# Kernel optimization log

Measured on AMD Instinct MI355X. Metric: run time of the kernel, lower is better.

## Reference

```python
import jax, jax.numpy as jnp
import numpy as np

B, V, F = 128, 256, 64      # batch, vertices, features-per-vertex
NS, NLR, K, NOUT = 4, 64, 40, 128
F_EFF = 2 * F               # cat_means doubles feature dim


def setup_inputs() -> dict:
    key = jax.random.key(0)
    k0, k1, k2 = jax.random.split(key, 3)
    x = jax.random.normal(k0, (B, V, F), dtype=jnp.float32)
    # f_slr: single Linear(F_EFF, NS+NLR) + ReLU (f_slr_depth=1)
    W_slr = jax.random.normal(k1, (F_EFF, NS + NLR), dtype=jnp.float32) / np.sqrt(F_EFF).astype(np.float32)
    b_slr = jnp.zeros((NS + NLR,), dtype=jnp.float32)
    # f_out: single Linear(F_EFF + 2*NLR, NOUT) + ReLU (f_out_depth=1, 2 agg methods)
    fin = F_EFF + 2 * NLR
    W_out = jax.random.normal(k2, (fin, NOUT), dtype=jnp.float32) / np.sqrt(fin).astype(np.float32)
    b_out = jnp.zeros((NOUT,), dtype=jnp.float32)
    return {"x": x, "W_slr": W_slr, "b_slr": b_slr, "W_out": W_out, "b_out": b_out}


def reference(x, W_slr, b_slr, W_out, b_out):
    # cat_means: append per-event feature means (broadcast over vertices)
    x = jnp.concatenate([x, jnp.broadcast_to(x.mean(axis=1, keepdims=True), x.shape)], axis=-1)  # (B,V,2F)
    slr = jax.nn.relu(x @ W_slr + b_slr)                    # (B,V,NS+NLR)
    s, lr = slr[..., :NS], slr[..., NS:]
    # pairwise squared distances in latent space (potential only needs d^2, so
    # we skip the sqrt: exp(-10*d^2) == exp(-10*d2), and kNN order is identical)
    diff = s[:, :, None, :] - s[:, None, :, :]              # (B,V,V,NS)
    d2 = jnp.sum(diff * diff, axis=-1)                      # (B,V,V)
    _, idx = jax.lax.top_k(-d2, K)                          # (B,V,K) k smallest (incl. self)
    d2k = jnp.take_along_axis(d2, idx, axis=2)              # (B,V,K)
    lr_nb = jax.vmap(lambda l, i: l[i])(lr, idx)            # (B,V,K,NLR)
    v = jnp.exp(-10.0 * d2k)                                # potential exp(-10 d^2)
    ft = lr_nb * v[..., None]                               # (B,V,K,NLR)
    fp = jnp.concatenate([x, ft.mean(axis=2), ft.max(axis=2)], axis=-1)  # (B,V,2F+2NLR)
    return jax.nn.relu(fp @ W_out + b_out)                  # (B,V,NOUT)
```

## Files before the change

kernel.cpp:

```cpp
#include <hip/hip_runtime.h>

constexpr int Bn = 128, Vn = 256, Fn = 64;
constexpr int NSLR = 68, NSn = 4, NLRn = 64;
constexpr int Kn = 40, NOUTn = 128;
constexpr int ROWS = Bn * Vn;
constexpr int KB2 = 192;

typedef __attribute__((ext_vector_type(8))) short short8;
typedef __attribute__((ext_vector_type(4))) float f32x4;

__device__ __forceinline__ int mbcnt64(unsigned long long m) {
  return __builtin_amdgcn_mbcnt_hi((unsigned)(m >> 32),
         __builtin_amdgcn_mbcnt_lo((unsigned)(m & 0xFFFFFFFFull), 0));
}
__device__ __forceinline__ unsigned short rneb(float v) {
  unsigned u = __float_as_uint(v);
  unsigned r = u + 0x7FFFu + ((u >> 16) & 1u);
  return (unsigned short)(r >> 16);
}
__device__ __forceinline__ float bf2f(unsigned short h) {
  return __uint_as_float(((unsigned)h) << 16);
}
#define GL_LDS(gp, lp) __builtin_amdgcn_global_load_lds( \
    (const __attribute__((address_space(1))) void*)(gp), \
    (__attribute__((address_space(3))) void*)(lp), 16, 0, 0)

__global__ __launch_bounds__(256) void kprep(
    const float* __restrict__ x,
    const float* __restrict__ W_slr, const float* __restrict__ b_slr,
    const float* __restrict__ W_out, const float* __restrict__ b_out,
    short* __restrict__ xhi, short* __restrict__ xlo,
    short* __restrict__ wt1h, short* __restrict__ wt1l, short* __restrict__ wt2,
    float* __restrict__ bias1, float* __restrict__ bias2) {
  const int blk = blockIdx.x, t = threadIdx.x;
  if (blk >= Bn) {
    const int col = blk - Bn;
    if (t < 64) {
      float val = (col < NSLR) ? W_slr[t * NSLR + col] : 0.f;
      unsigned short h = rneb(val);
      wt1h[col * 64 + t] = (short)h;
      wt1l[col * 64 + t] = (short)rneb(val - bf2f(h));
    } else {
      int k = t - 64;
      int row = (k < 64) ? k : 64 + k;
      wt2[col * KB2 + k] = (short)rneb(W_out[row * NOUTn + col]);
    }
    return;
  }
  const int b = blk;
  const int f4 = t & 15, vg = t >> 4;
  const float4* xb = (const float4*)(x + (size_t)b * 16384);
  float4 sum = make_float4(0.f, 0.f, 0.f, 0.f);
  for (int i = 0; i < 16; ++i) {
    int v = vg * 16 + i;
    float4 val = xb[v * 16 + f4];
    sum.x += val.x; sum.y += val.y; sum.z += val.z; sum.w += val.w;
    unsigned short h0 = rneb(val.x), h1 = rneb(val.y), h2 = rneb(val.z), h3 = rneb(val.w);
    short4 hi = {(short)h0, (short)h1, (short)h2, (short)h3};
    short4 lo = {(short)rneb(val.x - bf2f(h0)), (short)rneb(val.y - bf2f(h1)),
                 (short)rneb(val.z - bf2f(h2)), (short)rneb(val.w - bf2f(h3))};
    size_t o = (size_t)b * 4096 + v * 16 + f4;
    ((short4*)xhi)[o] = hi;
    ((short4*)xlo)[o] = lo;
  }
  __shared__ float4 ps[16][16];
  __shared__ float xms[64];
  ps[vg][f4] = sum;
  __syncthreads();
  if (t < 16) {
    float4 m = ps[0][t];
    for (int g = 1; g < 16; ++g) {
      float4 v = ps[g][t];
      m.x += v.x; m.y += v.y; m.z += v.z; m.w += v.w;
    }
    m.x *= (1.f / 256.f); m.y *= (1.f / 256.f); m.z *= (1.f / 256.f); m.w *= (1.f / 256.f);
    ((float4*)xms)[t] = m;
  }
  __syncthreads();
  if (t < 128) {
    float acc = b_out[t];
    for (int f = 0; f < 64; ++f) acc = fmaf(xms[f], W_out[(64 + f) * NOUTn + t], acc);
    bias2[b * 128 + t] = acc;
  } else {
    int c = t - 128;
    if (c < NSLR) {
      float acc = b_slr[c];
      for (int f = 0; f < 64; ++f) acc = fmaf(xms[f], W_slr[(64 + f) * NSLR + c], acc);
      bias1[b * 128 + c] = acc;
    }
  }
}

__global__ __launch_bounds__(256) void kgemm1(
    const short* __restrict__ xhi, const short* __restrict__ xlo,
    const short* __restrict__ wt1h, const short* __restrict__ wt1l,
    const float* __restrict__ bias1,
    float* __restrict__ s_ws, unsigned short* __restrict__ lr_bf) {
  __shared__ __align__(16) short Ah[4096], Al[4096], Bh[8192], Bl[1024];
  const int t = threadIdx.x, l = t & 63, w = t >> 6;
  const int wr = w >> 1, wc = w & 1;
  const int rowBase = blockIdx.x * 64;
  const int b = rowBase >> 8;
  const int lr8 = l >> 3, ul = (l & 7) ^ lr8;

#pragma unroll
  for (int rep = 0; rep < 2; ++rep) {
    const int seg = w + rep * 4;
    size_t o = (size_t)(rowBase + seg * 8 + lr8) * 64 + ul * 8;
    GL_LDS(xhi + o, &Ah[seg * 512]);
    GL_LDS(xlo + o, &Al[seg * 512]);
  }
#pragma unroll
  for (int rep = 0; rep < 4; ++rep) {
    const int seg = w + rep * 4;
    size_t o = (size_t)(seg * 8 + lr8) * 64 + ul * 8;
    GL_LDS(wt1h + o, &Bh[seg * 512]);
  }
  if (w < 2) {
    size_t o = (size_t)(w * 8 + lr8) * 64 + ul * 8;
    GL_LDS(wt1l + o, &Bl[w * 512]);
  }
  __syncthreads();

  f32x4 acc[2][4];
#pragma unroll
  for (int mf = 0; mf < 2; ++mf)
#pragma unroll
    for (int nf = 0; nf < 4; ++nf) acc[mf][nf] = (f32x4)(0.f);

#pragma unroll
  for (int ks = 0; ks < 2; ++ks) {
    short8 ah[2], bh[4];
#pragma unroll
    for (int mf = 0; mf < 2; ++mf) {
      int row = wr * 32 + mf * 16 + (l & 15);
      int pu = (ks * 4 + (l >> 4)) ^ (row & 7);
      ah[mf] = *(const short8*)&Ah[row * 64 + pu * 8];
    }
#pragma unroll
    for (int nf = 0; nf < 4; ++nf) {
      int col = wc * 64 + nf * 16 + (l & 15);
      int pu = (ks * 4 + (l >> 4)) ^ (col & 7);
      bh[nf] = *(const short8*)&Bh[col * 64 + pu * 8];
    }
#pragma unroll
    for (int mf = 0; mf < 2; ++mf)
#pragma unroll
      for (int nf = 0; nf < 4; ++nf)
        acc[mf][nf] = __builtin_amdgcn_mfma_f32_16x16x32_bf16(ah[mf], bh[nf], acc[mf][nf], 0, 0, 0);
    if (wc == 0) {
      int col0 = l & 15;
      int puc = (ks * 4 + (l >> 4)) ^ (col0 & 7);
      short8 bl0 = *(const short8*)&Bl[col0 * 64 + puc * 8];
#pragma unroll
      for (int mf = 0; mf < 2; ++mf) {
        int row = wr * 32 + mf * 16 + (l & 15);
        int pu = (ks * 4 + (l >> 4)) ^ (row & 7);
        short8 al = *(const short8*)&Al[row * 64 + pu * 8];
        acc[mf][0] = __builtin_amdgcn_mfma_f32_16x16x32_bf16(ah[mf], bl0, acc[mf][0], 0, 0, 0);
        acc[mf][0] = __builtin_amdgcn_mfma_f32_16x16x32_bf16(al, bh[0], acc[mf][0], 0, 0, 0);
      }
    }
  }
#pragma unroll
  for (int mf = 0; mf < 2; ++mf)
#pragma unroll
    for (int nf = 0; nf < 4; ++nf) {
      const int col = wc * 64 + nf * 16 + (l & 15);
      if (col < NSLR) {
        const float bia = bias1[b * 128 + col];
#pragma unroll
        for (int r = 0; r < 4; ++r) {
          int row = rowBase + wr * 32 + mf * 16 + (l >> 4) * 4 + r;
          float vv = acc[mf][nf][r] + bia;
          vv = vv > 0.f ? vv : 0.f;
          if (col < NSn) s_ws[b * 1024 + col * 256 + (row & 255)] = vv;
          else           lr_bf[(size_t)row * NLRn + (col - NSn)] = rneb(vv);
        }
      }
    }
}

__global__ __launch_bounds__(256) void kgemm2(
    const short* __restrict__ xhi, const short* __restrict__ fm,
    const short* __restrict__ fx, const short* __restrict__ wt2,
    const float* __restrict__ bias2, float* __restrict__ outp) {
  __shared__ __align__(16) short As[3][4096], Bs[3][8192];
  const int t = threadIdx.x, l = t & 63, w = t >> 6;
  const int wr = w >> 1, wc = w & 1;
  const int rowBase = blockIdx.x * 64;
  const int b = rowBase >> 8;
  const int lr8 = l >> 3, ul = (l & 7) ^ lr8;

#pragma unroll
  for (int kc = 0; kc < 3; ++kc) {
    const short* asrc = (kc == 0) ? xhi : (kc == 1) ? fm : fx;
#pragma unroll
    for (int rep = 0; rep < 2; ++rep) {
      const int seg = w + rep * 4;
      size_t o = (size_t)(rowBase + seg * 8 + lr8) * 64 + ul * 8;
      GL_LDS(asrc + o, &As[kc][seg * 512]);
    }
#pragma unroll
    for (int rep = 0; rep < 4; ++rep) {
      const int seg = w + rep * 4;
      size_t o = (size_t)(seg * 8 + lr8) * KB2 + kc * 64 + ul * 8;
      GL_LDS(wt2 + o, &Bs[kc][seg * 512]);
    }
  }
  __syncthreads();

  f32x4 acc[2][4];
#pragma unroll
  for (int mf = 0; mf < 2; ++mf)
#pragma unroll
    for (int nf = 0; nf < 4; ++nf) acc[mf][nf] = (f32x4)(0.f);

#pragma unroll
  for (int kc = 0; kc < 3; ++kc) {
#pragma unroll
    for (int ks = 0; ks < 2; ++ks) {
      short8 a[2], bb[4];
#pragma unroll
      for (int mf = 0; mf < 2; ++mf) {
        int row = wr * 32 + mf * 16 + (l & 15);
        int pu = (ks * 4 + (l >> 4)) ^ (row & 7);
        a[mf] = *(const short8*)&As[kc][row * 64 + pu * 8];
      }
#pragma unroll
      for (int nf = 0; nf < 4; ++nf) {
        int col = wc * 64 + nf * 16 + (l & 15);
        int pu = (ks * 4 + (l >> 4)) ^ (col & 7);
        bb[nf] = *(const short8*)&Bs[kc][col * 64 + pu * 8];
      }
#pragma unroll
      for (int mf = 0; mf < 2; ++mf)
#pragma unroll
        for (int nf = 0; nf < 4; ++nf)
          acc[mf][nf] = __builtin_amdgcn_mfma_f32_16x16x32_bf16(a[mf], bb[nf], acc[mf][nf], 0, 0, 0);
    }
  }
#pragma unroll
  for (int mf = 0; mf < 2; ++mf)
#pragma unroll
    for (int nf = 0; nf < 4; ++nf) {
      const int col = wc * 64 + nf * 16 + (l & 15);
      const float bia = bias2[b * 128 + col];
#pragma unroll
      for (int r = 0; r < 4; ++r) {
        int row = rowBase + wr * 32 + mf * 16 + (l >> 4) * 4 + r;
        float vv = acc[mf][nf][r] + bia;
        outp[(size_t)row * NOUTn + col] = vv > 0.f ? vv : 0.f;
      }
    }
}

__device__ __forceinline__ int cntlt(const unsigned* kbr, unsigned c) {
  return __popcll(__ballot(kbr[0] < c)) + __popcll(__ballot(kbr[1] < c)) +
         __popcll(__ballot(kbr[2] < c)) + __popcll(__ballot(kbr[3] < c));
}

__global__ __launch_bounds__(256) void kselect(const float* __restrict__ s_ws,
                                               const unsigned short* __restrict__ lr_bf,
                                               unsigned* __restrict__ fm32,
                                               unsigned* __restrict__ fx32) {
  __shared__ float sT[4][256];
  __shared__ __align__(16) unsigned short lrs[16384];
  __shared__ unsigned int lst[4][4][Kn];
  const int id = blockIdx.x;
  const int xcd = id & 7;
  const int rrx = id >> 3;
  const int b = xcd + 8 * (rrx & 15);
  const int seg = rrx >> 4;
  const int t = threadIdx.x, lane = t & 63, w = t >> 6;

  {
    const unsigned short* lrg = lr_bf + (size_t)b * (256 * NLRn);
#pragma unroll
    for (int it = 0; it < 8; ++it)
      GL_LDS(lrg + (it * 256 + t) * 8, &lrs[(it * 256 + t) * 8]);
    const float* sb = s_ws + b * 1024;
    sT[0][t] = sb[t]; sT[1][t] = sb[256 + t];
    sT[2][t] = sb[512 + t]; sT[3][t] = sb[768 + t];
  }
  __syncthreads();

  float sj[4][4];
#pragma unroll
  for (int q = 0; q < 4; ++q)
#pragma unroll
    for (int c = 0; c < 4; ++c) sj[q][c] = sT[c][q * 64 + lane];

  const float C = -14.4269504088896340736f;
  unsigned kb[4][4];
  float vv[4][4];
#pragma unroll
  for (int r = 0; r < 4; ++r) {
    const int i = seg * 16 + w * 4 + r;
    const float si0 = sT[0][i], si1 = sT[1][i], si2 = sT[2][i], si3 = sT[3][i];
#pragma unroll
    for (int q = 0; q < 4; ++q) {
      float d0 = sj[q][0] - si0;
      float d1 = sj[q][1] - si1;
      float d2_ = sj[q][2] - si2;
      float d3 = sj[q][3] - si3;
      float dd = ((d0 * d0 + d1 * d1) + d2_ * d2_) + d3 * d3;
      kb[r][q] = __float_as_uint(dd);
      vv[r][q] = exp2f(C * dd);
    }
  }
  unsigned T[4] = {0u, 0u, 0u, 0u};
#pragma unroll 1
  for (int bit = 30; bit >= 0; --bit) {
    const unsigned m = 1u << bit;
    unsigned c0 = T[0] | m, c1 = T[1] | m, c2 = T[2] | m, c3 = T[3] | m;
    int n0 = cntlt(kb[0], c0);
    int n1 = cntlt(kb[1], c1);
    int n2 = cntlt(kb[2], c2);
    int n3 = cntlt(kb[3], c3);
    T[0] = (n0 < Kn) ? c0 : T[0];
    T[1] = (n1 < Kn) ? c1 : T[1];
    T[2] = (n2 < Kn) ? c2 : T[2];
    T[3] = (n3 < Kn) ? c3 : T[3];
  }
#pragma unroll
  for (int r = 0; r < 4; ++r) {
    const unsigned Tr = T[r];
    int nlt = cntlt(kb[r], Tr);
    int rem = Kn - nlt;
    int base = 0, ecum = 0;
#pragma unroll
    for (int q = 0; q < 4; ++q) {
      bool lt = kb[r][q] < Tr;
      bool eq = kb[r][q] == Tr;
      unsigned long long meq = __ballot(eq);
      int eqrank = ecum + mbcnt64(meq);
      bool sel = lt || (eq && (eqrank < rem));
      unsigned long long msel = __ballot(sel);
      int pos = base + mbcnt64(msel);
      if (sel)
        lst[w][r][pos] = (__float_as_uint(vv[r][q]) & 0xFFFFFF00u) | (unsigned)(q * 64 + lane);
      base += __popcll(msel);
      ecum += __popcll(meq);
    }
  }
  const int h = lane >> 5;
  const int f2 = lane & 31;
#pragma unroll
  for (int p = 0; p < 2; ++p) {
    const unsigned* lstp = &lst[w][2 * p + h][0];
    float am0 = 0.f, am1 = 0.f, ax0 = 0.f, ax1 = 0.f;
#pragma unroll 4
    for (int tt = 0; tt < Kn; ++tt) {
      unsigned pk = lstp[tt];
      float v = __uint_as_float(pk & 0xFFFFFF00u);
      unsigned off = (pk & 0xFFu) << 6;
      unsigned pr = *(const unsigned*)&lrs[off + f2 * 2];
      float l0 = __uint_as_float(pr << 16);
      float l1 = __uint_as_float(pr & 0xFFFF0000u);
      float t0 = v * l0, t1 = v * l1;
      am0 += t0; am1 += t1;
      ax0 = fmaxf(ax0, t0); ax1 = fmaxf(ax1, t1);
    }
    const int i = seg * 16 + w * 4 + 2 * p + h;
    size_t ro = ((size_t)(b * 256 + i)) * 32 + f2;
    am0 *= (1.f / 40.f); am1 *= (1.f / 40.f);
    fm32[ro] = (unsigned)rneb(am0) | ((unsigned)rneb(am1) << 16);
    fx32[ro] = (unsigned)rneb(ax0) | ((unsigned)rneb(ax1) << 16);
  }
}

extern "C" void kernel_launch(void* const* d_in, const int* in_sizes, int n_in,
                              void* d_out, int out_size, void* d_ws, size_t ws_size,
                              hipStream_t stream) {
  const float* x = (const float*)d_in[0];
  const float* W_slr = (const float*)d_in[1];
  const float* b_slr = (const float*)d_in[2];
  const float* W_out = (const float*)d_in[3];
  const float* b_out = (const float*)d_in[4];
  float* out = (float*)d_out;

  char* p = (char*)d_ws;
  auto take = [&](size_t bytes) { char* c = p; p += (bytes + 255) & ~(size_t)255; return c; };
  short* xhi = (short*)take((size_t)ROWS * 64 * 2);
  short* xlo = (short*)take((size_t)ROWS * 64 * 2);
  short* wt1h = (short*)take(128 * 64 * 2);
  short* wt1l = (short*)take(128 * 64 * 2);
  short* wt2 = (short*)take(128 * KB2 * 2);
  float* bias1 = (float*)take(Bn * 128 * 4);
  float* bias2 = (float*)take(Bn * 128 * 4);
  float* s_ws = (float*)take(Bn * 1024 * 4);
  unsigned short* lr_bf = (unsigned short*)take((size_t)ROWS * 64 * 2);
  short* fm = (short*)take((size_t)ROWS * 64 * 2);
  short* fx = (short*)take((size_t)ROWS * 64 * 2);

  kprep<<<256, 256, 0, stream>>>(x, W_slr, b_slr, W_out, b_out,
                                 xhi, xlo, wt1h, wt1l, wt2, bias1, bias2);
  kgemm1<<<ROWS / 64, 256, 0, stream>>>(xhi, xlo, wt1h, wt1l, bias1, s_ws, lr_bf);
  kselect<<<Bn * 16, 256, 0, stream>>>(s_ws, lr_bf, (unsigned*)fm, (unsigned*)fx);
  kgemm2<<<ROWS / 64, 256, 0, stream>>>(xhi, fm, fx, wt2, bias2, out);
}
```

Baseline: 133.0 us.

## Process 8 query rows per wave in kselect and gather lr from global

Each wave now handles 8 query vertices instead of 4, which halves the grid and amortizes the per-block s loads and the radix-select loop over more rows. The per-block 32KB LDS staging of the batch's lr matrix is dropped, and the gather reads bf16 lr values directly from global memory through cache. The exp potential is now computed only in the selection loop rather than precomputed for all candidates. In exchange the kernel uses more registers per thread (kb[8][4]), issues scattered global gathers, and runs fewer blocks, which lowers occupancy and parallelism.

```diff
diff --git a/kernel.cpp b/kernel.cpp
--- a/kernel.cpp
+++ b/kernel.cpp
@@ -265,20 +265,15 @@
                                                unsigned* __restrict__ fm32,
                                                unsigned* __restrict__ fx32) {
   __shared__ float sT[4][256];
-  __shared__ __align__(16) unsigned short lrs[16384];
-  __shared__ unsigned int lst[4][4][Kn];
+  __shared__ unsigned int lst[4][8][Kn];
   const int id = blockIdx.x;
   const int xcd = id & 7;
-  const int rrx = id >> 3;
-  const int b = xcd + 8 * (rrx & 15);
-  const int seg = rrx >> 4;
+  const int k_ = id >> 3;
+  const int b = xcd + 8 * (k_ & 15);
+  const int seg = k_ >> 4;
   const int t = threadIdx.x, lane = t & 63, w = t >> 6;
 
   {
-    const unsigned short* lrg = lr_bf + (size_t)b * (256 * NLRn);
-#pragma unroll
-    for (int it = 0; it < 8; ++it)
-      GL_LDS(lrg + (it * 256 + t) * 8, &lrs[(it * 256 + t) * 8]);
     const float* sb = s_ws + b * 1024;
     sT[0][t] = sb[t]; sT[1][t] = sb[256 + t];
     sT[2][t] = sb[512 + t]; sT[3][t] = sb[768 + t];
@@ -292,11 +287,10 @@
     for (int c = 0; c < 4; ++c) sj[q][c] = sT[c][q * 64 + lane];
 
   const float C = -14.4269504088896340736f;
-  unsigned kb[4][4];
-  float vv[4][4];
-#pragma unroll
-  for (int r = 0; r < 4; ++r) {
-    const int i = seg * 16 + w * 4 + r;
+  unsigned kb[8][4];
+#pragma unroll
+  for (int r = 0; r < 8; ++r) {
+    const int i = seg * 32 + w * 8 + r;
     const float si0 = sT[0][i], si1 = sT[1][i], si2 = sT[2][i], si3 = sT[3][i];
 #pragma unroll
     for (int q = 0; q < 4; ++q) {
@@ -306,25 +300,23 @@
       float d3 = sj[q][3] - si3;
       float dd = ((d0 * d0 + d1 * d1) + d2_ * d2_) + d3 * d3;
       kb[r][q] = __float_as_uint(dd);
-      vv[r][q] = exp2f(C * dd);
-    }
-  }
-  unsigned T[4] = {0u, 0u, 0u, 0u};
+    }
+  }
+  unsigned T[8] = {0u, 0u, 0u, 0u, 0u, 0u, 0u, 0u};
 #pragma unroll 1
   for (int bit = 30; bit >= 0; --bit) {
     const unsigned m = 1u << bit;
-    unsigned c0 = T[0] | m, c1 = T[1] | m, c2 = T[2] | m, c3 = T[3] | m;
-    int n0 = cntlt(kb[0], c0);
-    int n1 = cntlt(kb[1], c1);
-    int n2 = cntlt(kb[2], c2);
-    int n3 = cntlt(kb[3], c3);
-    T[0] = (n0 < Kn) ? c0 : T[0];
-    T[1] = (n1 < Kn) ? c1 : T[1];
-    T[2] = (n2 < Kn) ? c2 : T[2];
-    T[3] = (n3 < Kn) ? c3 : T[3];
-  }
-#pragma unroll
-  for (int r = 0; r < 4; ++r) {
+    unsigned cnd[8];
+    int n[8];
+#pragma unroll
+    for (int r = 0; r < 8; ++r) cnd[r] = T[r] | m;
+#pragma unroll
+    for (int r = 0; r < 8; ++r) n[r] = cntlt(kb[r], cnd[r]);
+#pragma unroll
+    for (int r = 0; r < 8; ++r) T[r] = (n[r] < Kn) ? cnd[r] : T[r];
+  }
+#pragma unroll
+  for (int r = 0; r < 8; ++r) {
     const unsigned Tr = T[r];
     int nlt = cntlt(kb[r], Tr);
     int rem = Kn - nlt;
@@ -338,31 +330,32 @@
       bool sel = lt || (eq && (eqrank < rem));
       unsigned long long msel = __ballot(sel);
       int pos = base + mbcnt64(msel);
+      float v = exp2f(C * __uint_as_float(kb[r][q]));
       if (sel)
-        lst[w][r][pos] = (__float_as_uint(vv[r][q]) & 0xFFFFFF00u) | (unsigned)(q * 64 + lane);
+        lst[w][r][pos] = (__float_as_uint(v) & 0xFFFFFF00u) | (unsigned)(q * 64 + lane);
       base += __popcll(msel);
       ecum += __popcll(meq);
     }
   }
   const int h = lane >> 5;
   const int f2 = lane & 31;
-#pragma unroll
-  for (int p = 0; p < 2; ++p) {
+  const unsigned short* lrb = lr_bf + (size_t)b * (256 * NLRn);
+#pragma unroll
+  for (int p = 0; p < 4; ++p) {
     const unsigned* lstp = &lst[w][2 * p + h][0];
     float am0 = 0.f, am1 = 0.f, ax0 = 0.f, ax1 = 0.f;
 #pragma unroll 4
     for (int tt = 0; tt < Kn; ++tt) {
       unsigned pk = lstp[tt];
       float v = __uint_as_float(pk & 0xFFFFFF00u);
-      unsigned off = (pk & 0xFFu) << 6;
-      unsigned pr = *(const unsigned*)&lrs[off + f2 * 2];
+      unsigned pr = *(const unsigned*)(lrb + ((pk & 0xFFu) << 6) + f2 * 2);
       float l0 = __uint_as_float(pr << 16);
       float l1 = __uint_as_float(pr & 0xFFFF0000u);
       float t0 = v * l0, t1 = v * l1;
       am0 += t0; am1 += t1;
       ax0 = fmaxf(ax0, t0); ax1 = fmaxf(ax1, t1);
     }
-    const int i = seg * 16 + w * 4 + 2 * p + h;
+    const int i = seg * 32 + w * 8 + 2 * p + h;
     size_t ro = ((size_t)(b * 256 + i)) * 32 + f2;
     am0 *= (1.f / 40.f); am1 *= (1.f / 40.f);
     fm32[ro] = (unsigned)rneb(am0) | ((unsigned)rneb(am1) << 16);
@@ -397,6 +390,6 @@
   kprep<<<256, 256, 0, stream>>>(x, W_slr, b_slr, W_out, b_out,
                                  xhi, xlo, wt1h, wt1l, wt2, bias1, bias2);
   kgemm1<<<ROWS / 64, 256, 0, stream>>>(xhi, xlo, wt1h, wt1l, bias1, s_ws, lr_bf);
-  kselect<<<Bn * 16, 256, 0, stream>>>(s_ws, lr_bf, (unsigned*)fm, (unsigned*)fx);
+  kselect<<<Bn * 8, 256, 0, stream>>>(s_ws, lr_bf, (unsigned*)fm, (unsigned*)fx);
   kgemm2<<<ROWS / 64, 256, 0, stream>>>(xhi, fm, fx, wt2, bias2, out);
 }
```

After: 131.3 us. No clear change (-1.2%).

## Compute latent coords in fp32 in prep, drop hi/lo bf16 split, read lr from global

Applied to the files above, without the earlier changes.

Computes the 4 latent-space coordinates in exact fp32 inside the prep kernel, using an LDS copy of x. This lets the first GEMM drop the hi/lo bf16 split (no xlo buffer, no extra MFMAs) and compute only the 64 lr columns. The select kernel no longer stages the per-batch lr tile into LDS; it gathers lr directly from global/L2, interleaves the two rows' accumulation, and computes exp lazily. The risks are extra LDS (about 66KB) in kprep, which lowers occupancy, and uncached global gathers in kselect.

```diff
diff --git a/kernel.cpp b/kernel.cpp
--- a/kernel.cpp
+++ b/kernel.cpp
@@ -18,9 +18,6 @@
   unsigned r = u + 0x7FFFu + ((u >> 16) & 1u);
   return (unsigned short)(r >> 16);
 }
-__device__ __forceinline__ float bf2f(unsigned short h) {
-  return __uint_as_float(((unsigned)h) << 16);
-}
 #define GL_LDS(gp, lp) __builtin_amdgcn_global_load_lds( \
     (const __attribute__((address_space(1))) void*)(gp), \
     (__attribute__((address_space(3))) void*)(lp), 16, 0, 0)
@@ -29,17 +26,19 @@
     const float* __restrict__ x,
     const float* __restrict__ W_slr, const float* __restrict__ b_slr,
     const float* __restrict__ W_out, const float* __restrict__ b_out,
-    short* __restrict__ xhi, short* __restrict__ xlo,
-    short* __restrict__ wt1h, short* __restrict__ wt1l, short* __restrict__ wt2,
-    float* __restrict__ bias1, float* __restrict__ bias2) {
+    short* __restrict__ xhi, short* __restrict__ wt1, short* __restrict__ wt2,
+    float* __restrict__ bias1lr, float* __restrict__ bias2,
+    float* __restrict__ s_ws) {
   const int blk = blockIdx.x, t = threadIdx.x;
+  __shared__ float xs[256 * 65];
+  __shared__ float4 ps[16][16];
+  __shared__ float xms[64];
+  __shared__ float wss[256];
+  __shared__ float bS[4];
   if (blk >= Bn) {
     const int col = blk - Bn;
     if (t < 64) {
-      float val = (col < NSLR) ? W_slr[t * NSLR + col] : 0.f;
-      unsigned short h = rneb(val);
-      wt1h[col * 64 + t] = (short)h;
-      wt1l[col * 64 + t] = (short)rneb(val - bf2f(h));
+      if (col < 64) wt1[col * 64 + t] = (short)rneb(W_slr[t * NSLR + 4 + col]);
     } else {
       int k = t - 64;
       int row = (k < 64) ? k : 64 + k;
@@ -48,6 +47,7 @@
     return;
   }
   const int b = blk;
+  wss[t] = W_slr[(t >> 2) * NSLR + (t & 3)];
   const int f4 = t & 15, vg = t >> 4;
   const float4* xb = (const float4*)(x + (size_t)b * 16384);
   float4 sum = make_float4(0.f, 0.f, 0.f, 0.f);
@@ -55,16 +55,12 @@
     int v = vg * 16 + i;
     float4 val = xb[v * 16 + f4];
     sum.x += val.x; sum.y += val.y; sum.z += val.z; sum.w += val.w;
-    unsigned short h0 = rneb(val.x), h1 = rneb(val.y), h2 = rneb(val.z), h3 = rneb(val.w);
-    short4 hi = {(short)h0, (short)h1, (short)h2, (short)h3};
-    short4 lo = {(short)rneb(val.x - bf2f(h0)), (short)rneb(val.y - bf2f(h1)),
-                 (short)rneb(val.z - bf2f(h2)), (short)rneb(val.w - bf2f(h3))};
-    size_t o = (size_t)b * 4096 + v * 16 + f4;
-    ((short4*)xhi)[o] = hi;
-    ((short4*)xlo)[o] = lo;
-  }
-  __shared__ float4 ps[16][16];
-  __shared__ float xms[64];
+    short4 hi = {(short)rneb(val.x), (short)rneb(val.y),
+                 (short)rneb(val.z), (short)rneb(val.w)};
+    ((short4*)xhi)[(size_t)b * 4096 + v * 16 + f4] = hi;
+    float* xr = &xs[v * 65 + f4 * 4];
+    xr[0] = val.x; xr[1] = val.y; xr[2] = val.z; xr[3] = val.w;
+  }
   ps[vg][f4] = sum;
   __syncthreads();
   if (t < 16) {
@@ -81,22 +77,36 @@
     float acc = b_out[t];
     for (int f = 0; f < 64; ++f) acc = fmaf(xms[f], W_out[(64 + f) * NOUTn + t], acc);
     bias2[b * 128 + t] = acc;
-  } else {
+  } else if (t < 192) {
     int c = t - 128;
-    if (c < NSLR) {
-      float acc = b_slr[c];
-      for (int f = 0; f < 64; ++f) acc = fmaf(xms[f], W_slr[(64 + f) * NSLR + c], acc);
-      bias1[b * 128 + c] = acc;
-    }
-  }
+    float acc = b_slr[4 + c];
+    for (int f = 0; f < 64; ++f) acc = fmaf(xms[f], W_slr[(64 + f) * NSLR + 4 + c], acc);
+    bias1lr[b * 64 + c] = acc;
+  } else if (t < 196) {
+    int c = t - 192;
+    float acc = b_slr[c];
+    for (int f = 0; f < 64; ++f) acc = fmaf(xms[f], W_slr[(64 + f) * NSLR + c], acc);
+    bS[c] = acc;
+  }
+  __syncthreads();
+  float a0 = bS[0], a1 = bS[1], a2 = bS[2], a3 = bS[3];
+  for (int k = 0; k < 64; ++k) {
+    float xv = xs[t * 65 + k];
+    a0 = fmaf(xv, wss[k * 4 + 0], a0);
+    a1 = fmaf(xv, wss[k * 4 + 1], a1);
+    a2 = fmaf(xv, wss[k * 4 + 2], a2);
+    a3 = fmaf(xv, wss[k * 4 + 3], a3);
+  }
+  s_ws[b * 1024 + 0 * 256 + t] = fmaxf(a0, 0.f);
+  s_ws[b * 1024 + 1 * 256 + t] = fmaxf(a1, 0.f);
+  s_ws[b * 1024 + 2 * 256 + t] = fmaxf(a2, 0.f);
+  s_ws[b * 1024 + 3 * 256 + t] = fmaxf(a3, 0.f);
 }
 
 __global__ __launch_bounds__(256) void kgemm1(
-    const short* __restrict__ xhi, const short* __restrict__ xlo,
-    const short* __restrict__ wt1h, const short* __restrict__ wt1l,
-    const float* __restrict__ bias1,
-    float* __restrict__ s_ws, unsigned short* __restrict__ lr_bf) {
-  __shared__ __align__(16) short Ah[4096], Al[4096], Bh[8192], Bl[1024];
+    const short* __restrict__ xhi, const short* __restrict__ wt1,
+    const float* __restrict__ bias1lr, unsigned short* __restrict__ lr_bf) {
+  __shared__ __align__(16) short As[4096], Bs[4096];
   const int t = threadIdx.x, l = t & 63, w = t >> 6;
   const int wr = w >> 1, wc = w & 1;
   const int rowBase = blockIdx.x * 64;
@@ -106,77 +116,49 @@
 #pragma unroll
   for (int rep = 0; rep < 2; ++rep) {
     const int seg = w + rep * 4;
-    size_t o = (size_t)(rowBase + seg * 8 + lr8) * 64 + ul * 8;
-    GL_LDS(xhi + o, &Ah[seg * 512]);
-    GL_LDS(xlo + o, &Al[seg * 512]);
-  }
-#pragma unroll
-  for (int rep = 0; rep < 4; ++rep) {
-    const int seg = w + rep * 4;
-    size_t o = (size_t)(seg * 8 + lr8) * 64 + ul * 8;
-    GL_LDS(wt1h + o, &Bh[seg * 512]);
-  }
-  if (w < 2) {
-    size_t o = (size_t)(w * 8 + lr8) * 64 + ul * 8;
-    GL_LDS(wt1l + o, &Bl[w * 512]);
-  }
-  __syncthreads();
-
-  f32x4 acc[2][4];
+    GL_LDS(xhi + (size_t)(rowBase + seg * 8 + lr8) * 64 + ul * 8, &As[seg * 512]);
+    GL_LDS(wt1 + (size_t)(seg * 8 + lr8) * 64 + ul * 8, &Bs[seg * 512]);
+  }
+  __syncthreads();
+
+  f32x4 acc[2][2];
 #pragma unroll
   for (int mf = 0; mf < 2; ++mf)
 #pragma unroll
-    for (int nf = 0; nf < 4; ++nf) acc[mf][nf] = (f32x4)(0.f);
+    for (int nf = 0; nf < 2; ++nf) acc[mf][nf] = (f32x4)(0.f);
 
 #pragma unroll
   for (int ks = 0; ks < 2; ++ks) {
-    short8 ah[2], bh[4];
+    short8 a[2], bb[2];
 #pragma unroll
     for (int mf = 0; mf < 2; ++mf) {
       int row = wr * 32 + mf * 16 + (l & 15);
       int pu = (ks * 4 + (l >> 4)) ^ (row & 7);
-      ah[mf] = *(const short8*)&Ah[row * 64 + pu * 8];
-    }
-#pragma unroll
-    for (int nf = 0; nf < 4; ++nf) {
-      int col = wc * 64 + nf * 16 + (l & 15);
+      a[mf] = *(const short8*)&As[row * 64 + pu * 8];
+    }
+#pragma unroll
+    for (int nf = 0; nf < 2; ++nf) {
+      int col = wc * 32 + nf * 16 + (l & 15);
       int pu = (ks * 4 + (l >> 4)) ^ (col & 7);
-      bh[nf] = *(const short8*)&Bh[col * 64 + pu * 8];
+      bb[nf] = *(const short8*)&Bs[col * 64 + pu * 8];
     }
 #pragma unroll
     for (int mf = 0; mf < 2; ++mf)
 #pragma unroll
-      for (int nf = 0; nf < 4; ++nf)
-        acc[mf][nf] = __builtin_amdgcn_mfma_f32_16x16x32_bf16(ah[mf], bh[nf], acc[mf][nf], 0, 0, 0);
-    if (wc == 0) {
-      int col0 = l & 15;
-      int puc = (ks * 4 + (l >> 4)) ^ (col0 & 7);
-      short8 bl0 = *(const short8*)&Bl[col0 * 64 + puc * 8];
-#pragma unroll
-      for (int mf = 0; mf < 2; ++mf) {
-        int row = wr * 32 + mf * 16 + (l & 15);
-        int pu = (ks * 4 + (l >> 4)) ^ (row & 7);
-        short8 al = *(const short8*)&Al[row * 64 + pu * 8];
-        acc[mf][0] = __builtin_amdgcn_mfma_f32_16x16x32_bf16(ah[mf], bl0, acc[mf][0], 0, 0, 0);
-        acc[mf][0] = __builtin_amdgcn_mfma_f32_16x16x32_bf16(al, bh[0], acc[mf][0], 0, 0, 0);
-      }
-    }
+      for (int nf = 0; nf < 2; ++nf)
+        acc[mf][nf] = __builtin_amdgcn_mfma_f32_16x16x32_bf16(a[mf], bb[nf], acc[mf][nf], 0, 0, 0);
   }
 #pragma unroll
   for (int mf = 0; mf < 2; ++mf)
 #pragma unroll
-    for (int nf = 0; nf < 4; ++nf) {
-      const int col = wc * 64 + nf * 16 + (l & 15);
-      if (col < NSLR) {
-        const float bia = bias1[b * 128 + col];
-#pragma unroll
-        for (int r = 0; r < 4; ++r) {
-          int row = rowBase + wr * 32 + mf * 16 + (l >> 4) * 4 + r;
-          float vv = acc[mf][nf][r] + bia;
-          vv = vv > 0.f ? vv : 0.f;
-          if (col < NSn) s_ws[b * 1024 + col * 256 + (row & 255)] = vv;
-          else           lr_bf[(size_t)row * NLRn + (col - NSn)] = rneb(vv);
-        }
+    for (int nf = 0; nf < 2; ++nf) {
+      const int col = wc * 32 + nf * 16 + (l & 15);
+      const float bia = bias1lr[b * 64 + col];
+#pragma unroll
+      for (int r = 0; r < 4; ++r) {
+        int row = rowBase + wr * 32 + mf * 16 + (l >> 4) * 4 + r;
+        float vv = acc[mf][nf][r] + bia;
+        lr_bf[(size_t)row * NLRn + col] = rneb(vv > 0.f ? vv : 0.f);
       }
     }
 }
@@ -198,14 +180,12 @@
 #pragma unroll
     for (int rep = 0; rep < 2; ++rep) {
       const int seg = w + rep * 4;
-      size_t o = (size_t)(rowBase + seg * 8 + lr8) * 64 + ul * 8;
-      GL_LDS(asrc + o, &As[kc][seg * 512]);
+      GL_LDS(asrc + (size_t)(rowBase + seg * 8 + lr8) * 64 + ul * 8, &As[kc][seg * 512]);
     }
 #pragma unroll
     for (int rep = 0; rep < 4; ++rep) {
       const int seg = w + rep * 4;
-      size_t o = (size_t)(seg * 8 + lr8) * KB2 + kc * 64 + ul * 8;
-      GL_LDS(wt2 + o, &Bs[kc][seg * 512]);
+      GL_LDS(wt2 + (size_t)(seg * 8 + lr8) * KB2 + kc * 64 + ul * 8, &Bs[kc][seg * 512]);
     }
   }
   __syncthreads();
@@ -265,7 +245,6 @@
                                                unsigned* __restrict__ fm32,
                                                unsigned* __restrict__ fx32) {
   __shared__ float sT[4][256];
-  __shared__ __align__(16) unsigned short lrs[16384];
   __shared__ unsigned int lst[4][4][Kn];
   const int id = blockIdx.x;
   const int xcd = id & 7;
@@ -275,10 +254,6 @@
   const int t = threadIdx.x, lane = t & 63, w = t >> 6;
 
   {
-    const unsigned short* lrg = lr_bf + (size_t)b * (256 * NLRn);
-#pragma unroll
-    for (int it = 0; it < 8; ++it)
-      GL_LDS(lrg + (it * 256 + t) * 8, &lrs[(it * 256 + t) * 8]);
     const float* sb = s_ws + b * 1024;
     sT[0][t] = sb[t]; sT[1][t] = sb[256 + t];
     sT[2][t] = sb[512 + t]; sT[3][t] = sb[768 + t];
@@ -293,7 +268,6 @@
 
   const float C = -14.4269504088896340736f;
   unsigned kb[4][4];
-  float vv[4][4];
 #pragma unroll
   for (int r = 0; r < 4; ++r) {
     const int i = seg * 16 + w * 4 + r;
@@ -306,7 +280,6 @@
       float d3 = sj[q][3] - si3;
       float dd = ((d0 * d0 + d1 * d1) + d2_ * d2_) + d3 * d3;
       kb[r][q] = __float_as_uint(dd);
-      vv[r][q] = exp2f(C * dd);
     }
   }
   unsigned T[4] = {0u, 0u, 0u, 0u};
@@ -338,35 +311,39 @@
       bool sel = lt || (eq && (eqrank < rem));
       unsigned long long msel = __ballot(sel);
       int pos = base + mbcnt64(msel);
+      float v = exp2f(C * __uint_as_float(kb[r][q]));
       if (sel)
-        lst[w][r][pos] = (__float_as_uint(vv[r][q]) & 0xFFFFFF00u) | (unsigned)(q * 64 + lane);
+        lst[w][r][pos] = (__float_as_uint(v) & 0xFFFFFF00u) | (unsigned)(q * 64 + lane);
       base += __popcll(msel);
       ecum += __popcll(meq);
     }
   }
   const int h = lane >> 5;
   const int f2 = lane & 31;
-#pragma unroll
-  for (int p = 0; p < 2; ++p) {
-    const unsigned* lstp = &lst[w][2 * p + h][0];
-    float am0 = 0.f, am1 = 0.f, ax0 = 0.f, ax1 = 0.f;
+  const unsigned short* lrb = lr_bf + (size_t)b * (256 * NLRn);
+  float am0[2] = {0.f, 0.f}, am1[2] = {0.f, 0.f};
+  float ax0[2] = {0.f, 0.f}, ax1[2] = {0.f, 0.f};
 #pragma unroll 4
-    for (int tt = 0; tt < Kn; ++tt) {
-      unsigned pk = lstp[tt];
+  for (int tt = 0; tt < Kn; ++tt) {
+#pragma unroll
+    for (int p = 0; p < 2; ++p) {
+      unsigned pk = lst[w][2 * p + h][tt];
       float v = __uint_as_float(pk & 0xFFFFFF00u);
-      unsigned off = (pk & 0xFFu) << 6;
-      unsigned pr = *(const unsigned*)&lrs[off + f2 * 2];
+      unsigned pr = *(const unsigned*)(lrb + ((pk & 0xFFu) << 6) + f2 * 2);
       float l0 = __uint_as_float(pr << 16);
       float l1 = __uint_as_float(pr & 0xFFFF0000u);
       float t0 = v * l0, t1 = v * l1;
-      am0 += t0; am1 += t1;
-      ax0 = fmaxf(ax0, t0); ax1 = fmaxf(ax1, t1);
-    }
+      am0[p] += t0; am1[p] += t1;
+      ax0[p] = fmaxf(ax0[p], t0); ax1[p] = fmaxf(ax1[p], t1);
+    }
+  }
+#pragma unroll
+  for (int p = 0; p < 2; ++p) {
     const int i = seg * 16 + w * 4 + 2 * p + h;
     size_t ro = ((size_t)(b * 256 + i)) * 32 + f2;
-    am0 *= (1.f / 40.f); am1 *= (1.f / 40.f);
-    fm32[ro] = (unsigned)rneb(am0) | ((unsigned)rneb(am1) << 16);
-    fx32[ro] = (unsigned)rneb(ax0) | ((unsigned)rneb(ax1) << 16);
+    float m0 = am0[p] * (1.f / 40.f), m1 = am1[p] * (1.f / 40.f);
+    fm32[ro] = (unsigned)rneb(m0) | ((unsigned)rneb(m1) << 16);
+    fx32[ro] = (unsigned)rneb(ax0[p]) | ((unsigned)rneb(ax1[p]) << 16);
   }
 }
 
@@ -383,11 +360,9 @@
   char* p = (char*)d_ws;
   auto take = [&](size_t bytes) { char* c = p; p += (bytes + 255) & ~(size_t)255; return c; };
   short* xhi = (short*)take((size_t)ROWS * 64 * 2);
-  short* xlo = (short*)take((size_t)ROWS * 64 * 2);
-  short* wt1h = (short*)take(128 * 64 * 2);
-  short* wt1l = (short*)take(128 * 64 * 2);
+  short* wt1 = (short*)take(64 * 64 * 2);
   short* wt2 = (short*)take(128 * KB2 * 2);
-  float* bias1 = (float*)take(Bn * 128 * 4);
+  float* bias1lr = (float*)take(Bn * 64 * 4);
   float* bias2 = (float*)take(Bn * 128 * 4);
   float* s_ws = (float*)take(Bn * 1024 * 4);
   unsigned short* lr_bf = (unsigned short*)take((size_t)ROWS * 64 * 2);
@@ -395,8 +370,8 @@
   short* fx = (short*)take((size_t)ROWS * 64 * 2);
 
   kprep<<<256, 256, 0, stream>>>(x, W_slr, b_slr, W_out, b_out,
-                                 xhi, xlo, wt1h, wt1l, wt2, bias1, bias2);
-  kgemm1<<<ROWS / 64, 256, 0, stream>>>(xhi, xlo, wt1h, wt1l, bias1, s_ws, lr_bf);
+                                 xhi, wt1, wt2, bias1lr, bias2, s_ws);
+  kgemm1<<<ROWS / 64, 256, 0, stream>>>(xhi, wt1, bias1lr, lr_bf);
   kselect<<<Bn * 16, 256, 0, stream>>>(s_ws, lr_bf, (unsigned*)fm, (unsigned*)fx);
   kgemm2<<<ROWS / 64, 256, 0, stream>>>(xhi, fm, fx, wt2, bias2, out);
 }
```

After: 122.4 us. 1.09x faster.
